# Optimization experiments

Measured on AMD Instinct MI355X. Metric: run time of the kernel, lower is better.

The kernel has to match this reference:

```python
import jax, jax.numpy as jnp
import numpy as np

DT = 0.001  # seconds per step (keras_spiking default)
BATCH, SEQ, SIZE = 64, 1024, 512


def setup_inputs() -> dict:
    key = jax.random.key(0)
    k1, k2 = jax.random.split(key)
    inputs = jax.random.normal(k1, (BATCH, SEQ, SIZE), dtype=jnp.float32)
    initial_level = jnp.zeros((SIZE,), dtype=jnp.float32)
    # time constants around the 0.01s used in the docstring example
    tau = 0.005 + 0.05 * jax.random.uniform(k2, (SIZE,), dtype=jnp.float32)
    return {"inputs": inputs, "initial_level": initial_level, "tau": tau}


def _alpha_filter(inputs, initial_level, tau):
    # inputs: [B, T, K]; initial_level, tau: [K]
    B_, T, K = inputs.shape
    tau_c = jnp.maximum(tau, 1e-8)               # clip for stability (as in forward pass)
    dt_tau = DT / tau_c                           # [K]
    dt_tau2 = dt_tau / tau_c                      # [K]
    e = jnp.exp(-dt_tau)                          # [K]
    # per-feature 2x2 transition matrix A: [K, 2, 2]
    row0 = jnp.stack([1.0 - dt_tau, -dt_tau2], axis=-1)             # [K, 2]
    row1 = jnp.stack([DT * jnp.ones_like(tau_c), 1.0 + dt_tau], -1)  # [K, 2]
    A = e[:, None, None] * jnp.stack([row0, row1], axis=-2)          # [K, 2, 2]
    # input vector B: [K, 2]
    Bvec = jnp.stack([e * dt_tau2, 1.0 - e * (1.0 + dt_tau)], axis=-1)
    Bt = Bvec.T  # [2, K]
    # initial state: row 0 zeros, row 1 initial_level -> [B, 2, K]
    x0 = jnp.stack(
        [jnp.zeros((B_, K), inputs.dtype),
         jnp.broadcast_to(initial_level, (B_, K))], axis=1)

    def step(x, u):
        # x: [B, 2, K], u: [B, K]
        xn = jnp.einsum('kij,mjk->mik', A, x) + Bt[None, :, :] * u[:, None, :]
        return xn, xn[:, 1]  # output is second state component

    _, ys = jax.lax.scan(step, x0, jnp.swapaxes(inputs, 0, 1))  # ys: [T, B, K]
    return jnp.swapaxes(ys, 0, 1)  # [B, T, K]


def reference(inputs, initial_level, tau):
    return _alpha_filter(inputs, initial_level, tau)
```

## Files before the change

### kernel.cpp

```cpp
#include <hip/hip_runtime.h>
#include <math.h>

namespace {
constexpr int kB = 64;
constexpr int kT = 1024;
constexpr int kK = 512;
constexpr int kP = 32;
constexpr float kDT = 0.001f;
}

__global__ __launch_bounds__(64, 1) void alpha_scan(
    const float* __restrict__ in,
    const float* __restrict__ init_level,
    const float* __restrict__ tau,
    float* __restrict__ out)
{
    const int gid = blockIdx.x * blockDim.x + threadIdx.x;
    const int k = gid & (kK - 1);
    const int b = gid >> 9;

    const float tc      = fmaxf(tau[k], 1e-8f);
    const float dt_tau  = kDT / tc;
    const float dt_tau2 = dt_tau / tc;
    const float e       = expf(-dt_tau);

    const float a00 = e * (1.0f - dt_tau);
    const float a01 = e * (-dt_tau2);
    const float a10 = e * kDT;
    const float a11 = e * (1.0f + dt_tau);
    const float b0  = e * dt_tau2;
    const float b1  = 1.0f - e * (1.0f + dt_tau);

    float x0 = 0.0f;
    float x1 = init_level[k];

    const float* __restrict__ pin = in  + (size_t)b * kT * kK + k;
    float* __restrict__ pout      = out + (size_t)b * kT * kK + k;

    float buf[kP];
    #pragma unroll
    for (int i = 0; i < kP; ++i) buf[i] = pin[(size_t)i * kK];

    for (int tb = 0; tb < kT - kP; tb += kP) {
        const float* __restrict__ pld = pin  + (size_t)(tb + kP) * kK;
        float* __restrict__ pst       = pout + (size_t)tb * kK;
        #pragma unroll
        for (int i = 0; i < kP; ++i) {
            const float u = buf[i];
            buf[i] = pld[(size_t)i * kK];
            const float nx0 = fmaf(a00, x0, fmaf(a01, x1, b0 * u));
            const float nx1 = fmaf(a10, x0, fmaf(a11, x1, b1 * u));
            x0 = nx0; x1 = nx1;
            pst[(size_t)i * kK] = nx1;
        }
    }
    {
        float* __restrict__ pst = pout + (size_t)(kT - kP) * kK;
        #pragma unroll
        for (int i = 0; i < kP; ++i) {
            const float u = buf[i];
            const float nx0 = fmaf(a00, x0, fmaf(a01, x1, b0 * u));
            const float nx1 = fmaf(a10, x0, fmaf(a11, x1, b1 * u));
            x0 = nx0; x1 = nx1;
            pst[(size_t)i * kK] = nx1;
        }
    }
}

extern "C" void kernel_launch(void* const* d_in, const int* in_sizes, int n_in,
                              void* d_out, int out_size, void* d_ws, size_t ws_size,
                              hipStream_t stream) {
    const float* in  = (const float*)d_in[0];
    const float* il  = (const float*)d_in[1];
    const float* tau = (const float*)d_in[2];
    float* out = (float*)d_out;

    const int total = kB * kK;
    dim3 block(64);
    dim3 grid(total / 64);
    alpha_scan<<<grid, block, 0, stream>>>(in, il, tau, out);
}
```

Before: 236.2 us.

## Split time axis into chunks with two-pass chunked scan and matrix-power carry

Splits each sequence into 8 time chunks handled by separate wavefronts. Each chunk first runs the recurrence from a zero state, and the final states go to shared memory. A carry-in is then built from A^128 (computed by repeated squaring) and the earlier chunks' states, and each chunk rescans its inputs to write outputs. This exposes 8x more parallelism than the original 2048 single-wave serial scan. The cost is reading the input twice and a small rounding difference in the combined carry.

```diff
diff --git a/kernel.cpp b/kernel.cpp
--- a/kernel.cpp
+++ b/kernel.cpp
@@ -2,22 +2,30 @@
 #include <math.h>
 
 namespace {
-constexpr int kB = 64;
-constexpr int kT = 1024;
-constexpr int kK = 512;
-constexpr int kP = 32;
+constexpr int kB  = 64;
+constexpr int kT  = 1024;
+constexpr int kK  = 512;
+constexpr int kC  = 8;
+constexpr int kL  = kT / kC;
+constexpr int kKB = 64;
+constexpr int kPF = 8;
 constexpr float kDT = 0.001f;
 }
 
-__global__ __launch_bounds__(64, 1) void alpha_scan(
+__global__ __launch_bounds__(kKB * kC, 4) void alpha_scan2(
     const float* __restrict__ in,
     const float* __restrict__ init_level,
     const float* __restrict__ tau,
     float* __restrict__ out)
 {
-    const int gid = blockIdx.x * blockDim.x + threadIdx.x;
-    const int k = gid & (kK - 1);
-    const int b = gid >> 9;
+    __shared__ float sF0[kC][kKB];
+    __shared__ float sF1[kC][kKB];
+
+    const int lane = threadIdx.x & 63;
+    const int c    = threadIdx.x >> 6;
+    const int kg   = blockIdx.x & 7;
+    const int b    = blockIdx.x >> 3;
+    const int k    = kg * kKB + lane;
 
     const float tc      = fmaxf(tau[k], 1e-8f);
     const float dt_tau  = kDT / tc;
@@ -31,38 +39,84 @@
     const float b0  = e * dt_tau2;
     const float b1  = 1.0f - e * (1.0f + dt_tau);
 
-    float x0 = 0.0f;
-    float x1 = init_level[k];
+    const float* __restrict__ pin =
+        in + ((size_t)b * kT + (size_t)c * kL) * kK + k;
 
-    const float* __restrict__ pin = in  + (size_t)b * kT * kK + k;
-    float* __restrict__ pout      = out + (size_t)b * kT * kK + k;
-
-    float buf[kP];
-    #pragma unroll
-    for (int i = 0; i < kP; ++i) buf[i] = pin[(size_t)i * kK];
-
-    for (int tb = 0; tb < kT - kP; tb += kP) {
-        const float* __restrict__ pld = pin  + (size_t)(tb + kP) * kK;
-        float* __restrict__ pst       = pout + (size_t)tb * kK;
+    float x0 = 0.0f, x1 = 0.0f;
+    {
+        float buf[kPF];
         #pragma unroll
-        for (int i = 0; i < kP; ++i) {
+        for (int i = 0; i < kPF; ++i) buf[i] = pin[(size_t)i * kK];
+        for (int t0 = 0; t0 < kL - kPF; t0 += kPF) {
+            const float* __restrict__ pld = pin + (size_t)(t0 + kPF) * kK;
+            #pragma unroll
+            for (int i = 0; i < kPF; ++i) {
+                const float u = buf[i];
+                buf[i] = pld[(size_t)i * kK];
+                const float n0 = fmaf(a00, x0, fmaf(a01, x1, b0 * u));
+                const float n1 = fmaf(a10, x0, fmaf(a11, x1, b1 * u));
+                x0 = n0; x1 = n1;
+            }
+        }
+        #pragma unroll
+        for (int i = 0; i < kPF; ++i) {
             const float u = buf[i];
-            buf[i] = pld[(size_t)i * kK];
-            const float nx0 = fmaf(a00, x0, fmaf(a01, x1, b0 * u));
-            const float nx1 = fmaf(a10, x0, fmaf(a11, x1, b1 * u));
-            x0 = nx0; x1 = nx1;
-            pst[(size_t)i * kK] = nx1;
+            const float n0 = fmaf(a00, x0, fmaf(a01, x1, b0 * u));
+            const float n1 = fmaf(a10, x0, fmaf(a11, x1, b1 * u));
+            x0 = n0; x1 = n1;
         }
     }
+    sF0[c][lane] = x0;
+    sF1[c][lane] = x1;
+    __syncthreads();
+
+    float m00 = a00, m01 = a01, m10 = a10, m11 = a11;
+    #pragma unroll
+    for (int s = 0; s < 7; ++s) {
+        const float t00 = fmaf(m00, m00, m01 * m10);
+        const float t01 = fmaf(m00, m01, m01 * m11);
+        const float t10 = fmaf(m10, m00, m11 * m10);
+        const float t11 = fmaf(m10, m01, m11 * m11);
+        m00 = t00; m01 = t01; m10 = t10; m11 = t11;
+    }
+
+    float s0 = 0.0f, s1 = init_level[k];
+    for (int cp = 0; cp < c; ++cp) {
+        const float f0 = sF0[cp][lane];
+        const float f1 = sF1[cp][lane];
+        const float n0 = fmaf(m00, s0, fmaf(m01, s1, f0));
+        const float n1 = fmaf(m10, s0, fmaf(m11, s1, f1));
+        s0 = n0; s1 = n1;
+    }
+
+    x0 = s0; x1 = s1;
+    float* __restrict__ pout =
+        out + ((size_t)b * kT + (size_t)c * kL) * kK + k;
     {
-        float* __restrict__ pst = pout + (size_t)(kT - kP) * kK;
+        float buf[kPF];
         #pragma unroll
-        for (int i = 0; i < kP; ++i) {
+        for (int i = 0; i < kPF; ++i) buf[i] = pin[(size_t)i * kK];
+        for (int t0 = 0; t0 < kL - kPF; t0 += kPF) {
+            const float* __restrict__ pld = pin  + (size_t)(t0 + kPF) * kK;
+            float* __restrict__ pst       = pout + (size_t)t0 * kK;
+            #pragma unroll
+            for (int i = 0; i < kPF; ++i) {
+                const float u = buf[i];
+                buf[i] = pld[(size_t)i * kK];
+                const float n0 = fmaf(a00, x0, fmaf(a01, x1, b0 * u));
+                const float n1 = fmaf(a10, x0, fmaf(a11, x1, b1 * u));
+                x0 = n0; x1 = n1;
+                pst[(size_t)i * kK] = n1;
+            }
+        }
+        float* __restrict__ pst = pout + (size_t)(kL - kPF) * kK;
+        #pragma unroll
+        for (int i = 0; i < kPF; ++i) {
             const float u = buf[i];
-            const float nx0 = fmaf(a00, x0, fmaf(a01, x1, b0 * u));
-            const float nx1 = fmaf(a10, x0, fmaf(a11, x1, b1 * u));
-            x0 = nx0; x1 = nx1;
-            pst[(size_t)i * kK] = nx1;
+            const float n0 = fmaf(a00, x0, fmaf(a01, x1, b0 * u));
+            const float n1 = fmaf(a10, x0, fmaf(a11, x1, b1 * u));
+            x0 = n0; x1 = n1;
+            pst[(size_t)i * kK] = n1;
         }
     }
 }
@@ -75,8 +129,7 @@
     const float* tau = (const float*)d_in[2];
     float* out = (float*)d_out;
 
-    const int total = kB * kK;
-    dim3 block(64);
-    dim3 grid(total / 64);
-    alpha_scan<<<grid, block, 0, stream>>>(in, il, tau, out);
+    dim3 block(kKB * kC);
+    dim3 grid(kB * (kK / kKB));
+    alpha_scan2<<<grid, block, 0, stream>>>(in, il, tau, out);
 }
```

Result: slower. 253.8 us (+7.5%).
